# Performance work log

Hardware: AMD Instinct MI355X
Metric: run time of the kernel (lower is better)

Reference implementation:

```python
import jax, jax.numpy as jnp
import numpy as np
from jax import lax

ORDER = 6
WN = 0.5 / 50.0          # highpass_cutoff / (orig_fs/2)
UP, DOWN = 16, 25        # 64/100 reduced by gcd 4 (scipy resample_poly)
HALF_LEN = 10 * DOWN     # scipy kaiser half length = 10*max_rate
NTAPS = 2 * HALF_LEN + 1
PADLEN = 21              # sosfiltfilt default: 3*(2*n_sections+1), 3 biquads
CHANNELS = np.array([126, 125, 48, 112, 67, 93, 10, 61, 39, 108])
D_MODEL = 16
LN_EPS = 1e-5


def _butter_hp_sos(order, wn):
    # scipy.signal.butter(order, wn, btype='high', output='sos') in pure numpy
    fs = 2.0
    warped = 2.0 * fs * np.tan(np.pi * wn / fs)
    m = np.arange(-order + 1, order, 2)
    p = -np.exp(1j * np.pi * m / (2 * order))     # analog LP prototype poles
    k = np.real(1.0 / np.prod(-p))                # lp2hp gain (no zeros)
    p = warped / p                                # lp2hp poles; zeros at s=0
    z = np.zeros(order)
    fs2 = 2.0 * fs                                # bilinear, fs=2
    k = k * np.real(np.prod(fs2 - z) / np.prod(fs2 - p))
    z = (fs2 + z) / (fs2 - z)                     # digital zeros, all +1
    p = (fs2 + p) / (fs2 - p)
    pp = p[np.imag(p) > 0]
    pp = pp[np.argsort(-np.abs(np.abs(pp) - 1.0))]  # closest to unit circle last
    sos = []
    for i, pi in enumerate(pp):
        b = np.array([1.0, -2.0, 1.0]) * (k if i == 0 else 1.0)
        a = np.array([1.0, -2.0 * pi.real, np.abs(pi) ** 2])
        sos.append(np.concatenate([b, a]))
    return np.array(sos)


def _sosfilt_zi(sos):
    # scipy.signal.sosfilt_zi: steady-state of step response per section
    n = sos.shape[0]
    zi = np.zeros((n, 2))
    scale = 1.0
    for s in range(n):
        b0, b1, b2, _, a1, a2 = sos[s]
        A = np.array([[1.0 + a1, -1.0], [a2, 1.0]])
        B = np.array([b1 - a1 * b0, b2 - a2 * b0])
        zi[s] = scale * np.linalg.solve(A, B)
        scale *= (b0 + b1 + b2) / (1.0 + a1 + a2)
    return zi


SOS = _butter_hp_sos(ORDER, WN)
ZI = _sosfilt_zi(SOS)


def _resample_fir():
    # scipy firwin(2*half_len+1, 1/max_rate, window=('kaiser',5.0)) * up
    fc = 1.0 / DOWN
    m = np.arange(NTAPS) - (NTAPS - 1) / 2.0
    h = fc * np.sinc(fc * m) * np.kaiser(NTAPS, 5.0)
    h /= h.sum()
    return h * UP


H_BASE = _resample_fir()


def _pos_encoding(max_len, d):
    pos = np.arange(max_len)[:, None].astype(np.float64)
    div = np.exp(np.arange(0, d, 2) * (-np.log(10000.0) / d))
    pe = np.zeros((max_len, d))
    pe[:, 0::2] = np.sin(pos * div)
    pe[:, 1::2] = np.cos(pos * div)
    return pe.astype(np.float32)


PE = _pos_encoding(3840, D_MODEL)


def _sosfilt(x, zi):
    # x: (N,T), zi: (N,3,2). Cascade of biquads, transposed direct form II.
    sos = jnp.asarray(SOS, x.dtype)
    nsec = SOS.shape[0]

    def step(z, xt):
        v = xt
        zs = []
        for s in range(nsec):  # fixed tiny cascade, unrolled inside scan
            b0, b1, b2, a1, a2 = sos[s, 0], sos[s, 1], sos[s, 2], sos[s, 4], sos[s, 5]
            y = b0 * v + z[s][0]
            zs.append((b1 * v - a1 * y + z[s][1], b2 * v - a2 * y))
            v = y
        return tuple(zs), v

    z0 = tuple((zi[:, s, 0], zi[:, s, 1]) for s in range(nsec))
    _, y = lax.scan(step, z0, x.T)
    return y.T


def _sosfiltfilt(x):
    # scipy.signal.sosfiltfilt with default odd padding, padlen=21
    zi = jnp.asarray(ZI, x.dtype)
    front = 2.0 * x[:, :1] - x[:, PADLEN:0:-1]
    back = 2.0 * x[:, -1:] - x[:, -2:-PADLEN - 2:-1]
    ext = jnp.concatenate([front, x, back], axis=1)
    y = _sosfilt(ext, zi[None] * ext[:, 0, None, None])
    y = y[:, ::-1]
    y = _sosfilt(y, zi[None] * y[:, 0, None, None])
    return y[:, ::-1][:, PADLEN:-PADLEN]


def _resample_poly(x):
    # scipy.signal.resample_poly(x, 64, 100): upfirdn via dilated conv
    T = x.shape[-1]
    n_out = (T * UP) // DOWN + int((T * UP) % DOWN != 0)
    n_pre_pad = DOWN - HALF_LEN % DOWN
    n_pre_remove = (HALF_LEN + n_pre_pad) // DOWN

    def outlen(lh):
        return (((T - 1) * UP + lh) - 1) // DOWN + 1

    n_post = 0
    while outlen(NTAPS + n_pre_pad + n_post) < n_out + n_pre_remove:
        n_post += 1
    h = np.concatenate([np.zeros(n_pre_pad), H_BASE, np.zeros(n_post)])
    L = h.size
    rhs = jnp.asarray(h[::-1].copy(), x.dtype).reshape(1, 1, L)
    y = lax.conv_general_dilated(x[:, None, :], rhs, window_strides=(DOWN,),
                                 padding=[(L - 1, L - 1)], lhs_dilation=(UP,),
                                 dimension_numbers=('NCH', 'OIH', 'NCH'))
    return y[:, 0, n_pre_remove:n_pre_remove + n_out]


def _ln(x, g, b):
    mu = x.mean(-1, keepdims=True)
    var = ((x - mu) ** 2).mean(-1, keepdims=True)
    return (x - mu) * lax.rsqrt(var + LN_EPS) * g + b


def setup_inputs() -> dict:
    key = jax.random.key(0)
    ks = jax.random.split(key, 20)
    f32 = jnp.float32
    d = {
        'x': jax.random.normal(ks[0], (64, 128, 2000), f32),
        'conv_w': jax.random.normal(ks[1], (16, 10, 3), f32) * 0.15,
        'conv_b': jnp.zeros((16,), f32),
        'ln0_g': jnp.ones((16,), f32), 'ln0_b': jnp.zeros((16,), f32),
        'wqkv': jax.random.normal(ks[2], (48, 16), f32) * 0.125,
        'bqkv': jnp.zeros((48,), f32),
        'wo': jax.random.normal(ks[3], (16, 16), f32) * 0.25,
        'bo': jnp.zeros((16,), f32),
        'w1': jax.random.normal(ks[4], (32, 16), f32) * 0.2,
        'b1': jnp.zeros((32,), f32),
        'w2': jax.random.normal(ks[5], (16, 32), f32) * 0.2,
        'b2': jnp.zeros((16,), f32),
        'ln1_g': jnp.ones((16,), f32), 'ln1_b': jnp.zeros((16,), f32),
        'ln2_g': jnp.ones((16,), f32), 'ln2_b': jnp.zeros((16,), f32),
        'wfc': jax.random.normal(ks[6], (1, 16), f32) * 0.3,
        'bfc': jnp.zeros((1,), f32),
    }
    return d


def reference(x, conv_w, conv_b, ln0_g, ln0_b, wqkv, bqkv, wo, bo,
              w1, b1, w2, b2, ln1_g, ln1_b, ln2_g, ln2_b, wfc, bfc):
    B = x.shape[0]
    # remove Cz (last channel) then gather interesting channels
    x = x[:, :-1, :][:, jnp.asarray(CHANNELS), :]        # (B,10,T)
    x = x - x.mean(axis=1, keepdims=True)                # CAR
    C, T = x.shape[1], x.shape[2]
    xf = _sosfiltfilt(x.reshape(B * C, T))               # zero-phase highpass
    xr = _resample_poly(xf)                              # 100 Hz -> 64 Hz
    x = xr.reshape(B, C, -1)
    x = jnp.tanh(x)                                      # artifact_scale = 1.0
    mean = x.mean(axis=2, keepdims=True)                 # zscore, unbiased std
    var = ((x - mean) ** 2).sum(axis=2, keepdims=True) / (x.shape[2] - 1)
    std = jnp.maximum(jnp.sqrt(var), 1e-6)
    x = (x - mean) / std
    # conv1d k=3 pad=1 (10 -> 16) + relu
    x = lax.conv_general_dilated(x, conv_w, (1,), [(1, 1)],
                                 dimension_numbers=('NCH', 'OIH', 'NCH'))
    x = jax.nn.relu(x + conv_b[None, :, None])
    x = x.transpose(0, 2, 1)                             # (B,S,16)
    x = _ln(x, ln0_g, ln0_b)
    x = x + jnp.asarray(PE[:x.shape[1]], x.dtype)[None]
    # TransformerEncoderLayer, post-norm, nhead=1, relu FFN (eval: no dropout)
    qkv = x @ wqkv.T + bqkv
    q, k, v = jnp.split(qkv, 3, axis=-1)
    att = jax.nn.softmax(jnp.einsum('bqd,bkd->bqk', q, k) * 0.25, axis=-1)
    a = jnp.einsum('bqk,bkd->bqd', att, v) @ wo.T + bo
    x = _ln(x + a, ln1_g, ln1_b)
    f = jax.nn.relu(x @ w1.T + b1) @ w2.T + b2
    x = _ln(x + f, ln2_g, ln2_b)
    pooled = x.mean(axis=1)                              # adaptive avg pool -> 1
    return pooled @ wfc.T + bfc                          # (B,1)
```

## Files before the change

### kernel.cpp

```cpp
#include <hip/hip_runtime.h>
#include <cmath>
#include <complex>
#include <algorithm>

#ifndef M_PI
#define M_PI 3.14159265358979323846
#endif

typedef _Float16 f16x8 __attribute__((ext_vector_type(8)));
typedef _Float16 f16x4 __attribute__((ext_vector_type(4)));
typedef float f32x4 __attribute__((ext_vector_type(4)));

struct FiltArg {
  double b0[3], b1[3], b2[3], a1[3], a2[3];
  double zi0[3], zi1[3];
};
struct CorArg { double CA[16 * 6]; };
struct EigArg {
  double Pm[36], Pinv[36];
  double czi[6];
  double lam_re[3], lam_im[3];
  double lami_re[3], lami_im[3];
};
struct FirArg { float h[526]; };

static void design_sos(FiltArg& sa) {
  const int order = 6;
  const double wn = 0.5 / 50.0;
  const double fs = 2.0;
  double warped = 2.0 * fs * std::tan(M_PI * wn / fs);
  std::complex<double> p[6];
  for (int i = 0; i < order; i++) {
    int m = -order + 1 + 2 * i;
    p[i] = -std::exp(std::complex<double>(0.0, M_PI * m / (2.0 * order)));
  }
  std::complex<double> prod1(1, 0);
  for (int i = 0; i < 6; i++) prod1 *= -p[i];
  double k = (1.0 / prod1).real();
  for (int i = 0; i < 6; i++) p[i] = warped / p[i];
  const double fs2 = 2.0 * fs;
  std::complex<double> num(1, 0), den(1, 0);
  for (int i = 0; i < 6; i++) { num *= fs2; den *= (fs2 - p[i]); }
  k *= (num / den).real();
  for (int i = 0; i < 6; i++) p[i] = (fs2 + p[i]) / (fs2 - p[i]);
  std::complex<double> pp[3]; int n = 0;
  for (int i = 0; i < 6; i++) if (p[i].imag() > 0) pp[n++] = p[i];
  std::stable_sort(pp, pp + 3,
    [](const std::complex<double>& A, const std::complex<double>& B) {
      return std::fabs(std::abs(A) - 1.0) > std::fabs(std::abs(B) - 1.0);
    });
  double sos[3][6];
  for (int s = 0; s < 3; s++) {
    double g = (s == 0) ? k : 1.0;
    sos[s][0] = g; sos[s][1] = -2.0 * g; sos[s][2] = g;
    sos[s][3] = 1.0; sos[s][4] = -2.0 * pp[s].real(); sos[s][5] = std::norm(pp[s]);
  }
  double scale = 1.0;
  for (int s = 0; s < 3; s++) {
    double b0 = sos[s][0], b1 = sos[s][1], b2 = sos[s][2];
    double a1 = sos[s][4], a2 = sos[s][5];
    double det = 1.0 + a1 + a2;
    double r0 = b1 - a1 * b0, r1 = b2 - a2 * b0;
    double z0 = (r0 + r1) / det;
    double z1 = ((1.0 + a1) * r1 - a2 * r0) / det;
    sa.b0[s] = b0; sa.b1[s] = b1; sa.b2[s] = b2; sa.a1[s] = a1; sa.a2[s] = a2;
    sa.zi0[s] = scale * z0; sa.zi1[s] = scale * z1;
    scale *= (b0 + b1 + b2) / (1.0 + a1 + a2);
  }
}

static double host_step(const FiltArg& c, double z[6], double v) {
  for (int s = 0; s < 3; s++) {
    double y = c.b0[s] * v + z[2 * s];
    z[2 * s]     = c.b1[s] * v - c.a1[s] * y + z[2 * s + 1];
    z[2 * s + 1] = c.b2[s] * v - c.a2[s] * y;
    v = y;
  }
  return v;
}

static void build_filt(FiltArg& c, CorArg& co) {
  design_sos(c);
  for (int j = 0; j < 6; j++) {
    double z[6] = {0, 0, 0, 0, 0, 0};
    z[j] = 1.0;
    for (int i = 0; i < 16; i++) co.CA[i * 6 + j] = host_step(c, z, 0.0);
  }
}

static void build_eig(const FiltArg& c, EigArg& e) {
  double Pr[36];
  for (int s = 0; s < 3; s++) {
    double a1 = c.a1[s], a2 = c.a2[s];
    std::complex<double> disc = std::sqrt(std::complex<double>(a1 * a1 - 4.0 * a2, 0.0));
    std::complex<double> p = (-a1 + disc) / 2.0;
    if (p.imag() < 0) p = std::conj(p);
    std::complex<double> v[6] = {0, 0, 0, 0, 0, 0};
    v[2 * s] = 1.0;
    v[2 * s + 1] = a1 + p;
    std::complex<double> y = 1.0;
    for (int j = s + 1; j < 3; j++) {
      double b0j = c.b0[j], b1j = c.b1[j], b2j = c.b2[j];
      double a1j = c.a1[j], a2j = c.a2[j];
      std::complex<double> det = p * p + a1j * p + a2j;
      std::complex<double> r0 = (b1j - a1j * b0j) * y;
      std::complex<double> r1 = (b2j - a2j * b0j) * y;
      std::complex<double> z0 = (p * r0 + r1) / det;
      std::complex<double> z1 = ((p + a1j) * r1 - a2j * r0) / det;
      v[2 * j] = z0; v[2 * j + 1] = z1;
      y = b0j * y + z0;
    }
    for (int i = 0; i < 6; i++) {
      Pr[i * 6 + 2 * s]     = v[i].real();
      Pr[i * 6 + 2 * s + 1] = v[i].imag();
    }
    std::complex<double> lam = std::pow(p, 16);
    e.lam_re[s] = lam.real(); e.lam_im[s] = lam.imag();
    std::complex<double> li = 1.0 / lam;
    e.lami_re[s] = li.real(); e.lami_im[s] = li.imag();
  }
  for (int i = 0; i < 36; i++) e.Pm[i] = Pr[i];
  double M[6][12];
  for (int i = 0; i < 6; i++)
    for (int j = 0; j < 6; j++) { M[i][j] = Pr[i * 6 + j]; M[i][6 + j] = (i == j) ? 1.0 : 0.0; }
  for (int col = 0; col < 6; col++) {
    int piv = col;
    for (int i = col + 1; i < 6; i++)
      if (std::fabs(M[i][col]) > std::fabs(M[piv][col])) piv = i;
    if (piv != col) for (int j = 0; j < 12; j++) std::swap(M[col][j], M[piv][j]);
    double d = M[col][col];
    for (int j = 0; j < 12; j++) M[col][j] /= d;
    for (int i = 0; i < 6; i++) if (i != col) {
      double f = M[i][col];
      for (int j = 0; j < 12; j++) M[i][j] -= f * M[col][j];
    }
  }
  for (int i = 0; i < 6; i++)
    for (int j = 0; j < 6; j++) e.Pinv[i * 6 + j] = M[i][6 + j];
  double zv[6];
  for (int s = 0; s < 3; s++) { zv[2 * s] = c.zi0[s]; zv[2 * s + 1] = c.zi1[s]; }
  for (int i = 0; i < 6; i++) {
    double sum = 0.0;
    for (int j = 0; j < 6; j++) sum += e.Pinv[i * 6 + j] * zv[j];
    e.czi[i] = sum;
  }
}

static double bessel_i0(double x) {
  double s = 1.0, t = 1.0;
  for (int k = 1; k < 64; k++) {
    double u = x / (2.0 * k);
    t *= u * u; s += t;
    if (t < 1e-18 * s) break;
  }
  return s;
}

static void design_fir(FirArg& fa) {
  double h[501];
  const double fc = 1.0 / 25.0;
  double denom = bessel_i0(5.0);
  double sum = 0.0;
  for (int nn = 0; nn < 501; nn++) {
    double m = nn - 250.0;
    double xx = fc * m;
    double snc = (nn == 250) ? 1.0 : std::sin(M_PI * xx) / (M_PI * xx);
    double r = (2.0 * nn) / 500.0 - 1.0;
    double w = bessel_i0(5.0 * std::sqrt(std::max(0.0, 1.0 - r * r))) / denom;
    h[nn] = fc * snc * w; sum += h[nn];
  }
  for (int nn = 0; nn < 25; nn++) fa.h[nn] = 0.0f;
  for (int nn = 0; nn < 501; nn++) fa.h[25 + nn] = (float)(h[nn] / sum * 16.0);
}

__device__ inline double waveReduceSum(double v) {
  #pragma unroll
  for (int off = 32; off > 0; off >>= 1) v += __shfl_down(v, off, 64);
  return v;
}

__device__ inline void cpow_int(double br, double bi, int n, double& rr_, double& ri_) {
  double rr = 1.0, ri = 0.0;
  while (n) {
    if (n & 1) { double t = rr * br - ri * bi; ri = rr * bi + ri * br; rr = t; }
    double t2 = br * br - bi * bi; bi = 2.0 * br * bi; br = t2;
    n >>= 1;
  }
  rr_ = rr; ri_ = ri;
}

__global__ __launch_bounds__(256) void k_chansel_pe(const float* __restrict__ x,
                                                    float* __restrict__ xs,
                                                    float* __restrict__ pe,
                                                    float* __restrict__ out) {
  int gid = blockIdx.x;
  if (gid < 500) {
    int idx = gid * 256 + threadIdx.x;
    int b = idx / 2000, t = idx % 2000;
    const int ch[10] = {126, 125, 48, 112, 67, 93, 10, 61, 39, 108};
    const float* xb = x + (size_t)b * 128 * 2000;
    float v[10]; float s = 0.f;
    #pragma unroll
    for (int c = 0; c < 10; c++) { v[c] = xb[ch[c] * 2000 + t]; s += v[c]; }
    s *= 0.1f;
    #pragma unroll
    for (int c = 0; c < 10; c++) xs[((size_t)b * 10 + c) * 2000 + t] = v[c] - s;
  } else {
    int i = (gid - 500) * 256 + threadIdx.x;
    int t = i >> 4, d = i & 15, j = d >> 1;
    double div = exp(-((double)(2 * j)) * 0.5756462732485114);
    double a = (double)t * div;
    pe[i] = (float)((d & 1) ? cos(a) : sin(a));
    if (gid == 579 && threadIdx.x < 64) out[threadIdx.x] = 0.f;
  }
}

#define XR(t) xr[(t) + ((t) >> 5)]
#define YF(t) yf[(t) + ((t) >> 5)]
__global__ __launch_bounds__(128) void k_filtfilt(float* __restrict__ xs,
                                                  FiltArg c, CorArg co, EigArg eg) {
  __shared__ float xr[2112];
  __shared__ double yf[2112];
  __shared__ double wsum[3][2];
  int r = blockIdx.x;
  int gk = threadIdx.x;
  int lane = gk & 63;
  int wv = gk >> 6;
  float* x = xs + (size_t)r * 2000;

  float x0f = x[0], xlf = x[1999];
  for (int t = gk; t < 2048; t += 128) {
    float v;
    if (t < 21)        v = 2.f * x0f - x[21 - t];
    else if (t < 2021) v = x[t - 21];
    else if (t < 2042) v = 2.f * xlf - x[4019 - t];
    else               v = 0.f;
    XR(t) = v;
  }
  __syncthreads();

  double b0[3], b1[3], b2[3], a1[3], a2[3];
  #pragma unroll
  for (int s = 0; s < 3; s++) {
    b0[s] = c.b0[s]; b1[s] = c.b1[s]; b2[s] = c.b2[s];
    a1[s] = c.a1[s]; a2[s] = c.a2[s];
  }
  auto step = [&](double* z, double v) -> double {
    #pragma unroll
    for (int s = 0; s < 3; s++) {
      double y = b0[s] * v + z[2 * s];
      z[2 * s]     = b1[s] * v - a1[s] * y + z[2 * s + 1];
      z[2 * s + 1] = b2[s] * v - a2[s] * y;
      v = y;
    }
    return v;
  };

  auto eigscan = [&](double seed, const double* F, double* zst) {
    double G[6];
    #pragma unroll
    for (int i = 0; i < 6; i++) {
      double s = 0.0;
      #pragma unroll
      for (int j = 0; j < 6; j++) s += eg.Pinv[i * 6 + j] * F[j];
      G[i] = s;
    }
    double tre[3], tim[3], sre[3], sim[3];
    #pragma unroll
    for (int s3 = 0; s3 < 3; s3++) {
      double gre = G[2 * s3], gim = -G[2 * s3 + 1];
      double mre, mim;
      cpow_int(eg.lami_re[s3], eg.lami_im[s3], gk, mre, mim);
      tre[s3] = mre * gre - mim * gim;
      tim[s3] = mre * gim + mim * gre;
      double pr = tre[s3], pi = tim[s3];
      #pragma unroll
      for (int off = 1; off < 64; off <<= 1) {
        double ore = __shfl_up(pr, off, 64);
        double oim = __shfl_up(pi, off, 64);
        pr += (lane >= off) ? ore : 0.0;
        pi += (lane >= off) ? oim : 0.0;
      }
      sre[s3] = pr; sim[s3] = pi;
      if (wv == 0 && lane == 63) { wsum[s3][0] = pr; wsum[s3][1] = pi; }
    }
    __syncthreads();
    double coord[6];
    #pragma unroll
    for (int s3 = 0; s3 < 3; s3++) {
      double inc_re = sre[s3] + (wv ? wsum[s3][0] : 0.0);
      double inc_im = sim[s3] + (wv ? wsum[s3][1] : 0.0);
      double Sre = inc_re - tre[s3], Sim = inc_im - tim[s3];
      double c0re = seed * eg.czi[2 * s3];
      double c0im = -seed * eg.czi[2 * s3 + 1];
      double lkre, lkim;
      cpow_int(eg.lam_re[s3], eg.lam_im[s3], gk, lkre, lkim);
      double lm1re = lkre * eg.lami_re[s3] - lkim * eg.lami_im[s3];
      double lm1im = lkre * eg.lami_im[s3] + lkim * eg.lami_re[s3];
      if (gk == 0) { lm1re = 0.0; lm1im = 0.0; }
      double cre = lkre * c0re - lkim * c0im + lm1re * Sre - lm1im * Sim;
      double cim = lkre * c0im + lkim * c0re + lm1re * Sim + lm1im * Sre;
      coord[2 * s3] = cre;
      coord[2 * s3 + 1] = -cim;
    }
    #pragma unroll
    for (int i = 0; i < 6; i++) {
      double s = 0.0;
      #pragma unroll
      for (int j = 0; j < 6; j++) s += eg.Pm[i * 6 + j] * coord[j];
      zst[i] = s;
    }
  };

  int t0 = gk * 16;
  double z[6], yreg[16], zst[6];

  #pragma unroll
  for (int i = 0; i < 6; i++) z[i] = 0.0;
  for (int i = 0; i < 16; i++) yreg[i] = step(z, (double)XR(t0 + i));
  eigscan((double)XR(0), z, zst);
  for (int i = 0; i < 16; i++) {
    double corr = 0.0;
    #pragma unroll
    for (int j = 0; j < 6; j++) corr += co.CA[i * 6 + j] * zst[j];
    YF(t0 + i) = yreg[i] + corr;
  }
  __syncthreads();

  auto rin = [&](int j) -> double { return (j <= 2041) ? YF(2041 - j) : 0.0; };
  double seedB = YF(2041);
  #pragma unroll
  for (int i = 0; i < 6; i++) z[i] = 0.0;
  for (int i = 0; i < 16; i++) yreg[i] = step(z, rin(t0 + i));
  eigscan(seedB, z, zst);
  for (int i = 0; i < 16; i++) {
    int j = t0 + i;
    if (j >= 21 && j <= 2020) {
      double corr = 0.0;
      #pragma unroll
      for (int jj = 0; jj < 6; jj++) corr += co.CA[i * 6 + jj] * zst[jj];
      x[2020 - j] = (float)(yreg[i] + corr);
    }
  }
}

__global__ __launch_bounds__(256) void k_resample_norm(const float* __restrict__ xf,
                                                       float* __restrict__ xn,
                                                       FirArg fa) {
  __shared__ float xl[2000];
  __shared__ float hl[526];
  int r = blockIdx.x;
  const float* x = xf + (size_t)r * 2000;
  for (int i = threadIdx.x; i < 2000; i += 256) xl[i] = x[i];
  for (int i = threadIdx.x; i < 526; i += 256) hl[i] = fa.h[i];
  __syncthreads();
  float vals[5];
  #pragma unroll
  for (int kk = 0; kk < 5; kk++) {
    int o = threadIdx.x + kk * 256;
    int P = 25 * (o + 11);
    int phase = P & 15;
    float acc = 0.f;
    for (int m = phase; m <= 525; m += 16) {
      int idx = (P - m) >> 4;
      if (idx >= 0 && idx < 2000) acc += hl[m] * xl[idx];
    }
    vals[kk] = tanhf(acc);
  }
  double s = 0.0, ss = 0.0;
  #pragma unroll
  for (int kk = 0; kk < 5; kk++) {
    s += (double)vals[kk]; ss += (double)vals[kk] * (double)vals[kk];
  }
  s = waveReduceSum(s); ss = waveReduceSum(ss);
  __shared__ double red[8];
  int wid = threadIdx.x >> 6, lane = threadIdx.x & 63;
  if (lane == 0) { red[wid] = s; red[4 + wid] = ss; }
  __syncthreads();
  double S = red[0] + red[1] + red[2] + red[3];
  double SS = red[4] + red[5] + red[6] + red[7];
  double mean = S / 1280.0;
  double var = (SS - 1280.0 * mean * mean) / 1279.0;
  double sd = fmax(sqrt(fmax(var, 0.0)), 1e-6);
  float fmean = (float)mean, finv = (float)(1.0 / sd);
  #pragma unroll
  for (int kk = 0; kk < 5; kk++)
    xn[(size_t)r * 1280 + threadIdx.x + kk * 256] = (vals[kk] - fmean) * finv;
}

__global__ __launch_bounds__(256) void k_conv_ln_pe_qkv(const float* __restrict__ xn,
    const float* __restrict__ cw, const float* __restrict__ cb,
    const float* __restrict__ g0, const float* __restrict__ bt0,
    const float* __restrict__ wqkv, const float* __restrict__ bqkv,
    const float* __restrict__ pe,
    float* __restrict__ x0, float* __restrict__ Q,
    _Float16* __restrict__ Kp, _Float16* __restrict__ Vt_g) {
  __shared__ float w[480], bias[16], gg[16], gb[16];
  __shared__ float wq[768], bq[48];
  for (int i = threadIdx.x; i < 480; i += 256) w[i] = cw[i];
  for (int i = threadIdx.x; i < 768; i += 256) wq[i] = wqkv[i];
  if (threadIdx.x < 16) {
    bias[threadIdx.x] = cb[threadIdx.x];
    gg[threadIdx.x] = g0[threadIdx.x];
    gb[threadIdx.x] = bt0[threadIdx.x];
  }
  if (threadIdx.x < 48) bq[threadIdx.x] = bqkv[threadIdx.x];
  __syncthreads();
  int idx = blockIdx.x * 256 + threadIdx.x;
  int b = idx / 1280, t = idx % 1280;
  const float* xb = xn + (size_t)b * 10 * 1280;
  float in[10][3];
  #pragma unroll
  for (int i = 0; i < 10; i++)
    #pragma unroll
    for (int k = 0; k < 3; k++) {
      int tt = t - 1 + k;
      in[i][k] = (tt >= 0 && tt < 1280) ? xb[i * 1280 + tt] : 0.f;
    }
  float o[16];
  #pragma unroll
  for (int oc = 0; oc < 16; oc++) {
    float a = bias[oc];
    #pragma unroll
    for (int i = 0; i < 10; i++)
      #pragma unroll
      for (int k = 0; k < 3; k++) a += in[i][k] * w[oc * 30 + i * 3 + k];
    o[oc] = fmaxf(a, 0.f);
  }
  float mu = 0.f;
  #pragma unroll
  for (int d = 0; d < 16; d++) mu += o[d];
  mu *= (1.f / 16.f);
  float var = 0.f;
  #pragma unroll
  for (int d = 0; d < 16; d++) { float dd = o[d] - mu; var += dd * dd; }
  var *= (1.f / 16.f);
  float inv = 1.f / sqrtf(var + 1e-5f);
  float xv[16];
  float* outp = x0 + (size_t)idx * 16;
  const float* pep = pe + t * 16;
  #pragma unroll
  for (int d = 0; d < 16; d++) {
    xv[d] = (o[d] - mu) * inv * gg[d] + gb[d] + pep[d];
    outp[d] = xv[d];
  }
  float* qp = Q + (size_t)idx * 16;
  #pragma unroll
  for (int j = 0; j < 16; j++) {
    float a = bq[j];
    #pragma unroll
    for (int d = 0; d < 16; d++) a += xv[d] * wq[j * 16 + d];
    qp[j] = a;
  }
  {
    _Float16* kp = Kp + (size_t)idx * 32;
    #pragma unroll
    for (int j = 0; j < 16; j++) {
      float a = bq[16 + j];
      #pragma unroll
      for (int d = 0; d < 16; d++) a += xv[d] * wq[(16 + j) * 16 + d];
      kp[j] = (_Float16)a;
    }
    f16x8 zz;
    #pragma unroll
    for (int j = 0; j < 8; j++) zz[j] = (_Float16)0.f;
    *(f16x8*)&kp[16] = zz;
    *(f16x8*)&kp[24] = zz;
  }
  {
    _Float16* vt = Vt_g + (size_t)b * 16 * 1280 + t;
    #pragma unroll
    for (int j = 0; j < 16; j++) {
      float a = bq[32 + j];
      #pragma unroll
      for (int d = 0; d < 16; d++) a += xv[d] * wq[(32 + j) * 16 + d];
      vt[j * 1280] = (_Float16)a;
    }
  }
}

#define ATT_SHIFT 12.0f
__global__ __launch_bounds__(256) void k_attn_combine(const float* __restrict__ Q,
    const _Float16* __restrict__ Kp, const _Float16* __restrict__ Vt_g,
    const float* __restrict__ x0,
    const float* __restrict__ wo, const float* __restrict__ bo,
    const float* __restrict__ w1, const float* __restrict__ b1,
    const float* __restrict__ w2, const float* __restrict__ b2,
    const float* __restrict__ g1, const float* __restrict__ bb1,
    const float* __restrict__ g2, const float* __restrict__ bb2,
    const float* __restrict__ wfc, const float* __restrict__ bfc,
    float* __restrict__ out) {
  __shared__ __align__(16) _Float16 Ks2[64 * 32];
  __shared__ __align__(16) _Float16 Vt[16 * 72];
  __shared__ __align__(16) _Float16 Pld[4][16 * 40];
  __shared__ float Aly[64][17];
  __shared__ float swo[256], sw1[512], sw2[512];
  __shared__ float sbo[16], sb1[32], sb2[16], sg1[16], sbb1[16], sg2[16], sbb2[16];
  __shared__ float swf[16];
  int tid = threadIdx.x;
  int b  = blockIdx.x / 20;
  int rg = blockIdx.x % 20;
  int wv = tid >> 6;
  int lane = tid & 63;
  int col = lane & 15;
  int quad = lane >> 4;
  size_t base = (size_t)b * 1280;
  int row0 = rg * 64 + wv * 16;

  swo[tid] = wo[tid];
  for (int i = tid; i < 512; i += 256) { sw1[i] = w1[i]; sw2[i] = w2[i]; }
  if (tid < 16) {
    sbo[tid] = bo[tid]; sb2[tid] = b2[tid];
    sg1[tid] = g1[tid]; sbb1[tid] = bb1[tid];
    sg2[tid] = g2[tid]; sbb2[tid] = bb2[tid];
    swf[tid] = wfc[tid];
  }
  if (tid < 32) sb1[tid] = b1[tid];

  f16x8 qf;
  #pragma unroll
  for (int j = 0; j < 8; j++) qf[j] = (_Float16)0.f;
  if (quad < 2) {
    const float* qp = Q + (base + row0 + col) * 16 + quad * 8;
    #pragma unroll
    for (int j = 0; j < 8; j++) qf[j] = (_Float16)(0.25f * qp[j]);
  }
  f32x4 oacc = {0.f, 0.f, 0.f, 0.f};
  float lacc = 0.f;

  const _Float16* vt_b = Vt_g + (size_t)b * 16 * 1280;

  for (int s = 0; s < 20; s++) {
    __syncthreads();
    *(f16x8*)&Ks2[tid * 8] =
        *(const f16x8*)(Kp + (base + s * 64) * 32 + tid * 8);
    if (tid < 128) {
      int d = tid >> 3, qc = tid & 7;
      *(f16x8*)&Vt[d * 72 + qc * 8] =
          *(const f16x8*)(vt_b + d * 1280 + s * 64 + qc * 8);
    }
    __syncthreads();
    #pragma unroll
    for (int c = 0; c < 2; c++) {
      #pragma unroll
      for (int t = 0; t < 2; t++) {
        int keyoff = c * 32 + t * 16;
        f16x8 af = *(f16x8*)&Ks2[(keyoff + col) * 32 + quad * 8];
        f32x4 sf = {0.f, 0.f, 0.f, 0.f};
        sf = __builtin_amdgcn_mfma_f32_16x16x32_f16(af, qf, sf, 0, 0, 0);
        f16x4 ph;
        float psum = 0.f;
        #pragma unroll
        for (int r = 0; r < 4; r++) {
          float p = __expf(sf[r] - ATT_SHIFT);
          psum += p;
          ph[r] = (_Float16)p;
        }
        lacc += psum;
        *(f16x4*)&Pld[wv][col * 40 + t * 16 + quad * 4] = ph;
      }
      __syncthreads();
      f16x8 pf = *(f16x8*)&Pld[wv][col * 40 + quad * 8];
      f16x8 vf = *(f16x8*)&Vt[col * 72 + c * 32 + quad * 8];
      oacc = __builtin_amdgcn_mfma_f32_16x16x32_f16(pf, vf, oacc, 0, 0, 0);
      __syncthreads();
    }
  }
  lacc += __shfl_xor(lacc, 16, 64);
  lacc += __shfl_xor(lacc, 32, 64);
  #pragma unroll
  for (int r = 0; r < 4; r++) {
    float lr = __shfl(lacc, quad * 4 + r, 64);
    Aly[wv * 16 + quad * 4 + r][col] = oacc[r] / lr;
  }
  __syncthreads();

  if (tid < 64) {
    int grow = rg * 64 + tid;
    size_t goff = (base + grow) * 16;
    float a[16];
    #pragma unroll
    for (int d = 0; d < 16; d++) a[d] = Aly[tid][d];
    float h[16];
    const float* xr = x0 + goff;
    #pragma unroll
    for (int d = 0; d < 16; d++) {
      float o = sbo[d];
      #pragma unroll
      for (int e = 0; e < 16; e++) o += a[e] * swo[d * 16 + e];
      h[d] = xr[d] + o;
    }
    float mu = 0.f;
    #pragma unroll
    for (int d = 0; d < 16; d++) mu += h[d];
    mu *= (1.f / 16.f);
    float var = 0.f;
    #pragma unroll
    for (int d = 0; d < 16; d++) { float dd = h[d] - mu; var += dd * dd; }
    var *= (1.f / 16.f);
    float inv = 1.f / sqrtf(var + 1e-5f);
    float x1[16];
    #pragma unroll
    for (int d = 0; d < 16; d++) x1[d] = (h[d] - mu) * inv * sg1[d] + sbb1[d];
    float t1[32];
    #pragma unroll
    for (int j = 0; j < 32; j++) {
      float u = sb1[j];
      #pragma unroll
      for (int d = 0; d < 16; d++) u += x1[d] * sw1[j * 16 + d];
      t1[j] = fmaxf(u, 0.f);
    }
    float h2[16];
    #pragma unroll
    for (int d = 0; d < 16; d++) {
      float u = sb2[d];
      #pragma unroll
      for (int j = 0; j < 32; j++) u += t1[j] * sw2[d * 32 + j];
      h2[d] = x1[d] + u;
    }
    mu = 0.f;
    #pragma unroll
    for (int d = 0; d < 16; d++) mu += h2[d];
    mu *= (1.f / 16.f);
    var = 0.f;
    #pragma unroll
    for (int d = 0; d < 16; d++) { float dd = h2[d] - mu; var += dd * dd; }
    var *= (1.f / 16.f);
    inv = 1.f / sqrtf(var + 1e-5f);
    float pv = 0.f;
    #pragma unroll
    for (int d = 0; d < 16; d++)
      pv += ((h2[d] - mu) * inv * sg2[d] + sbb2[d]) * swf[d];
    double part = waveReduceSum((double)pv);
    if (tid == 0) {
      float add = (float)(part / 1280.0);
      if (blockIdx.x % 20 == 0) add += bfc[0];
      atomicAdd(&out[b], add);
    }
  }
}

extern "C" void kernel_launch(void* const* d_in, const int* in_sizes, int n_in,
                              void* d_out, int out_size, void* d_ws, size_t ws_size,
                              hipStream_t stream) {
  const float* x    = (const float*)d_in[0];
  const float* cw   = (const float*)d_in[1];
  const float* cb   = (const float*)d_in[2];
  const float* g0   = (const float*)d_in[3];
  const float* bt0  = (const float*)d_in[4];
  const float* wqkv = (const float*)d_in[5];
  const float* bqkv = (const float*)d_in[6];
  const float* wo   = (const float*)d_in[7];
  const float* bo   = (const float*)d_in[8];
  const float* w1   = (const float*)d_in[9];
  const float* b1   = (const float*)d_in[10];
  const float* w2   = (const float*)d_in[11];
  const float* b2   = (const float*)d_in[12];
  const float* g1   = (const float*)d_in[13];
  const float* bb1  = (const float*)d_in[14];
  const float* g2   = (const float*)d_in[15];
  const float* bb2  = (const float*)d_in[16];
  const float* wfc  = (const float*)d_in[17];
  const float* bfc  = (const float*)d_in[18];
  float* out = (float*)d_out;

  float* ws = (float*)d_ws;
  float* xs = ws;
  float* y1 = xs + 1280000;
  float* xn = y1 + 1306880;
  float* x0 = xn + 819200;
  float* Q  = x0 + 1310720;
  _Float16* Kp   = (_Float16*)(Q + 1310720);
  _Float16* Vt_g = (_Float16*)(Q + 2621440);
  float* pe = Q + 2621440 + 655360;

  FiltArg fc; CorArg co; EigArg eg; FirArg fa;
  build_filt(fc, co);
  build_eig(fc, eg);
  design_fir(fa);

  k_chansel_pe<<<580, 256, 0, stream>>>(x, xs, pe, out);
  k_filtfilt<<<640, 128, 0, stream>>>(xs, fc, co, eg);
  k_resample_norm<<<640, 256, 0, stream>>>(xs, xn, fa);
  k_conv_ln_pe_qkv<<<320, 256, 0, stream>>>(xn, cw, cb, g0, bt0, wqkv, bqkv,
                                            pe, x0, Q, Kp, Vt_g);
  k_attn_combine<<<1280, 256, 0, stream>>>(Q, Kp, Vt_g, x0, wo, bo, w1, b1,
                                           w2, b2, g1, bb1, g2, bb2, wfc, bfc,
                                           out);
}
```

Before: 230.8 us.

## Load attention K/V fragments directly from global and drop block barriers

Each wave now reads its K and V MFMA fragments straight from global memory into registers instead of staging them through shared memory with block-wide barriers. The four score MFMAs per 64-key tile are issued together, and the per-wave P buffer is widened so all four chunks are written before the PV MFMAs, so none of the barriers inside the loop are needed. This removes the synchronisation and LDS staging cost, but each wave now loads K/V redundantly from global or L2, and the P tile is written and read within a wave without an explicit barrier.

```diff
diff --git a/kernel.cpp b/kernel.cpp
--- a/kernel.cpp
+++ b/kernel.cpp
@@ -490,9 +490,7 @@
     const float* __restrict__ g2, const float* __restrict__ bb2,
     const float* __restrict__ wfc, const float* __restrict__ bfc,
     float* __restrict__ out) {
-  __shared__ __align__(16) _Float16 Ks2[64 * 32];
-  __shared__ __align__(16) _Float16 Vt[16 * 72];
-  __shared__ __align__(16) _Float16 Pld[4][16 * 40];
+  __shared__ __align__(16) _Float16 Pld[4][16 * 72];
   __shared__ float Aly[64][17];
   __shared__ float swo[256], sw1[512], sw2[512];
   __shared__ float sbo[16], sb1[32], sb2[16], sg1[16], sbb1[16], sg2[16], sbb2[16];
@@ -528,42 +526,53 @@
   f32x4 oacc = {0.f, 0.f, 0.f, 0.f};
   float lacc = 0.f;
 
+  const _Float16* kp_b = Kp + base * 32;
   const _Float16* vt_b = Vt_g + (size_t)b * 16 * 1280;
+  _Float16* pld = &Pld[wv][0];
+
+  f16x8 af0, af1, af2, af3;
+  #pragma unroll
+  for (int j = 0; j < 8; j++) {
+    af0[j] = (_Float16)0.f; af1[j] = (_Float16)0.f;
+    af2[j] = (_Float16)0.f; af3[j] = (_Float16)0.f;
+  }
 
   for (int s = 0; s < 20; s++) {
-    __syncthreads();
-    *(f16x8*)&Ks2[tid * 8] =
-        *(const f16x8*)(Kp + (base + s * 64) * 32 + tid * 8);
-    if (tid < 128) {
-      int d = tid >> 3, qc = tid & 7;
-      *(f16x8*)&Vt[d * 72 + qc * 8] =
-          *(const f16x8*)(vt_b + d * 1280 + s * 64 + qc * 8);
-    }
-    __syncthreads();
+    const _Float16* kt = kp_b + (size_t)s * 64 * 32;
+    if (quad < 2) {
+      af0 = *(const f16x8*)(kt + (col     ) * 32 + quad * 8);
+      af1 = *(const f16x8*)(kt + (col + 16) * 32 + quad * 8);
+      af2 = *(const f16x8*)(kt + (col + 32) * 32 + quad * 8);
+      af3 = *(const f16x8*)(kt + (col + 48) * 32 + quad * 8);
+    }
+    f16x8 vf0 = *(const f16x8*)(vt_b + col * 1280 + s * 64      + quad * 8);
+    f16x8 vf1 = *(const f16x8*)(vt_b + col * 1280 + s * 64 + 32 + quad * 8);
+
+    f32x4 sc[4];
+    #pragma unroll
+    for (int ch = 0; ch < 4; ch++) { sc[ch][0]=0.f; sc[ch][1]=0.f; sc[ch][2]=0.f; sc[ch][3]=0.f; }
+    sc[0] = __builtin_amdgcn_mfma_f32_16x16x32_f16(af0, qf, sc[0], 0, 0, 0);
+    sc[1] = __builtin_amdgcn_mfma_f32_16x16x32_f16(af1, qf, sc[1], 0, 0, 0);
+    sc[2] = __builtin_amdgcn_mfma_f32_16x16x32_f16(af2, qf, sc[2], 0, 0, 0);
+    sc[3] = __builtin_amdgcn_mfma_f32_16x16x32_f16(af3, qf, sc[3], 0, 0, 0);
+
+    #pragma unroll
+    for (int ch = 0; ch < 4; ch++) {
+      f16x4 ph; float psum = 0.f;
+      #pragma unroll
+      for (int r = 0; r < 4; r++) {
+        float p = __expf(sc[ch][r] - ATT_SHIFT);
+        psum += p;
+        ph[r] = (_Float16)p;
+      }
+      lacc += psum;
+      *(f16x4*)&pld[col * 72 + ch * 16 + quad * 4] = ph;
+    }
     #pragma unroll
     for (int c = 0; c < 2; c++) {
-      #pragma unroll
-      for (int t = 0; t < 2; t++) {
-        int keyoff = c * 32 + t * 16;
-        f16x8 af = *(f16x8*)&Ks2[(keyoff + col) * 32 + quad * 8];
-        f32x4 sf = {0.f, 0.f, 0.f, 0.f};
-        sf = __builtin_amdgcn_mfma_f32_16x16x32_f16(af, qf, sf, 0, 0, 0);
-        f16x4 ph;
-        float psum = 0.f;
-        #pragma unroll
-        for (int r = 0; r < 4; r++) {
-          float p = __expf(sf[r] - ATT_SHIFT);
-          psum += p;
-          ph[r] = (_Float16)p;
-        }
-        lacc += psum;
-        *(f16x4*)&Pld[wv][col * 40 + t * 16 + quad * 4] = ph;
-      }
-      __syncthreads();
-      f16x8 pf = *(f16x8*)&Pld[wv][col * 40 + quad * 8];
-      f16x8 vf = *(f16x8*)&Vt[col * 72 + c * 32 + quad * 8];
-      oacc = __builtin_amdgcn_mfma_f32_16x16x32_f16(pf, vf, oacc, 0, 0, 0);
-      __syncthreads();
+      f16x8 pf = *(f16x8*)&pld[col * 72 + c * 32 + quad * 8];
+      oacc = __builtin_amdgcn_mfma_f32_16x16x32_f16(pf, (c == 0) ? vf0 : vf1,
+                                                    oacc, 0, 0, 0);
     }
   }
   lacc += __shfl_xor(lacc, 16, 64);
```

New measurement: 243.0 us. +5.3%, slower.

## Split attention keys across waves with 32x32 MFMA and register-prefetched K/V

Applied to the files above, without the earlier changes.

Attention is restructured so each of the four waves covers all 64 query rows of the block but only a quarter of the keys. Scores come from 32x32x16 MFMAs, and K/V fragments are read straight from global memory into registers with one-step prefetch, replacing the shared-memory staging and the block-wide barriers. Partial outputs and row sums are then reduced across waves through shared memory. Q is now stored pre-scaled in fp16 and K is stored unpadded (16 halves per row instead of 32), which halves the K traffic and drops the zero-fill writes. The cost is more shared memory per block (larger P buffers plus per-wave partial outputs), which may lower occupancy.

```diff
diff --git a/kernel.cpp b/kernel.cpp
--- a/kernel.cpp
+++ b/kernel.cpp
@@ -10,6 +10,7 @@
 typedef _Float16 f16x8 __attribute__((ext_vector_type(8)));
 typedef _Float16 f16x4 __attribute__((ext_vector_type(4)));
 typedef float f32x4 __attribute__((ext_vector_type(4)));
+typedef float f32x16 __attribute__((ext_vector_type(16)));
 
 struct FiltArg {
   double b0[3], b1[3], b2[3], a1[3], a2[3];
@@ -393,7 +394,7 @@
     const float* __restrict__ g0, const float* __restrict__ bt0,
     const float* __restrict__ wqkv, const float* __restrict__ bqkv,
     const float* __restrict__ pe,
-    float* __restrict__ x0, float* __restrict__ Q,
+    float* __restrict__ x0, _Float16* __restrict__ Qh,
     _Float16* __restrict__ Kp, _Float16* __restrict__ Vt_g) {
   __shared__ float w[480], bias[16], gg[16], gb[16];
   __shared__ float wq[768], bq[48];
@@ -444,16 +445,16 @@
     xv[d] = (o[d] - mu) * inv * gg[d] + gb[d] + pep[d];
     outp[d] = xv[d];
   }
-  float* qp = Q + (size_t)idx * 16;
+  _Float16* qh = Qh + (size_t)idx * 16;
   #pragma unroll
   for (int j = 0; j < 16; j++) {
     float a = bq[j];
     #pragma unroll
     for (int d = 0; d < 16; d++) a += xv[d] * wq[j * 16 + d];
-    qp[j] = a;
+    qh[j] = (_Float16)(0.25f * a);
   }
   {
-    _Float16* kp = Kp + (size_t)idx * 32;
+    _Float16* kp = Kp + (size_t)idx * 16;
     #pragma unroll
     for (int j = 0; j < 16; j++) {
       float a = bq[16 + j];
@@ -461,11 +462,6 @@
       for (int d = 0; d < 16; d++) a += xv[d] * wq[(16 + j) * 16 + d];
       kp[j] = (_Float16)a;
     }
-    f16x8 zz;
-    #pragma unroll
-    for (int j = 0; j < 8; j++) zz[j] = (_Float16)0.f;
-    *(f16x8*)&kp[16] = zz;
-    *(f16x8*)&kp[24] = zz;
   }
   {
     _Float16* vt = Vt_g + (size_t)b * 16 * 1280 + t;
@@ -480,7 +476,7 @@
 }
 
 #define ATT_SHIFT 12.0f
-__global__ __launch_bounds__(256) void k_attn_combine(const float* __restrict__ Q,
+__global__ __launch_bounds__(256) void k_attn_combine(const _Float16* __restrict__ Qh,
     const _Float16* __restrict__ Kp, const _Float16* __restrict__ Vt_g,
     const float* __restrict__ x0,
     const float* __restrict__ wo, const float* __restrict__ bo,
@@ -490,10 +486,9 @@
     const float* __restrict__ g2, const float* __restrict__ bb2,
     const float* __restrict__ wfc, const float* __restrict__ bfc,
     float* __restrict__ out) {
-  __shared__ __align__(16) _Float16 Ks2[64 * 32];
-  __shared__ __align__(16) _Float16 Vt[16 * 72];
-  __shared__ __align__(16) _Float16 Pld[4][16 * 40];
-  __shared__ float Aly[64][17];
+  __shared__ __align__(16) _Float16 Pld[4][64 * 40];
+  __shared__ float AlyW[4][64][17];
+  __shared__ float Lly[4][64];
   __shared__ float swo[256], sw1[512], sw2[512];
   __shared__ float sbo[16], sb1[32], sb2[16], sg1[16], sbb1[16], sg2[16], sbb2[16];
   __shared__ float swf[16];
@@ -502,10 +497,12 @@
   int rg = blockIdx.x % 20;
   int wv = tid >> 6;
   int lane = tid & 63;
+  int l31 = lane & 31;
+  int lh = lane >> 5;
   int col = lane & 15;
   int quad = lane >> 4;
   size_t base = (size_t)b * 1280;
-  int row0 = rg * 64 + wv * 16;
+  int qrow0 = rg * 64;
 
   swo[tid] = wo[tid];
   for (int i = tid; i < 512; i += 256) { sw1[i] = w1[i]; sw2[i] = w2[i]; }
@@ -517,70 +514,85 @@
   }
   if (tid < 32) sb1[tid] = b1[tid];
 
-  f16x8 qf;
-  #pragma unroll
-  for (int j = 0; j < 8; j++) qf[j] = (_Float16)0.f;
-  if (quad < 2) {
-    const float* qp = Q + (base + row0 + col) * 16 + quad * 8;
-    #pragma unroll
-    for (int j = 0; j < 8; j++) qf[j] = (_Float16)(0.25f * qp[j]);
-  }
-  f32x4 oacc = {0.f, 0.f, 0.f, 0.f};
-  float lacc = 0.f;
-
+  f16x8 qf0 = *(const f16x8*)(Qh + (base + qrow0 + l31) * 16 + lh * 8);
+  f16x8 qf1 = *(const f16x8*)(Qh + (base + qrow0 + 32 + l31) * 16 + lh * 8);
+
+  const _Float16* kp_b = Kp + base * 16;
   const _Float16* vt_b = Vt_g + (size_t)b * 16 * 1280;
-
-  for (int s = 0; s < 20; s++) {
-    __syncthreads();
-    *(f16x8*)&Ks2[tid * 8] =
-        *(const f16x8*)(Kp + (base + s * 64) * 32 + tid * 8);
-    if (tid < 128) {
-      int d = tid >> 3, qc = tid & 7;
-      *(f16x8*)&Vt[d * 72 + qc * 8] =
-          *(const f16x8*)(vt_b + d * 1280 + s * 64 + qc * 8);
-    }
-    __syncthreads();
-    #pragma unroll
-    for (int c = 0; c < 2; c++) {
-      #pragma unroll
-      for (int t = 0; t < 2; t++) {
-        int keyoff = c * 32 + t * 16;
-        f16x8 af = *(f16x8*)&Ks2[(keyoff + col) * 32 + quad * 8];
-        f32x4 sf = {0.f, 0.f, 0.f, 0.f};
-        sf = __builtin_amdgcn_mfma_f32_16x16x32_f16(af, qf, sf, 0, 0, 0);
-        f16x4 ph;
-        float psum = 0.f;
+  int key0 = wv * 320;
+  _Float16* pld = &Pld[wv][0];
+
+  f32x4 oacc[4];
+  #pragma unroll
+  for (int mp = 0; mp < 4; mp++) { oacc[mp][0]=0.f; oacc[mp][1]=0.f; oacc[mp][2]=0.f; oacc[mp][3]=0.f; }
+  float lacc0 = 0.f, lacc1 = 0.f;
+
+  f16x8 afc0 = *(const f16x8*)(kp_b + (size_t)(key0 + l31) * 16 + lh * 8);
+  f16x8 afc1 = *(const f16x8*)(kp_b + (size_t)(key0 + 32 + l31) * 16 + lh * 8);
+  f16x8 vfc0 = *(const f16x8*)(vt_b + (size_t)col * 1280 + key0 + quad * 8);
+  f16x8 vfc1 = *(const f16x8*)(vt_b + (size_t)col * 1280 + key0 + 32 + quad * 8);
+
+  for (int t = 0; t < 5; t++) {
+    f16x8 afn0, afn1, vfn0, vfn1;
+    if (t < 4) {
+      int nk = key0 + (t + 1) * 64;
+      afn0 = *(const f16x8*)(kp_b + (size_t)(nk + l31) * 16 + lh * 8);
+      afn1 = *(const f16x8*)(kp_b + (size_t)(nk + 32 + l31) * 16 + lh * 8);
+      vfn0 = *(const f16x8*)(vt_b + (size_t)col * 1280 + nk + quad * 8);
+      vfn1 = *(const f16x8*)(vt_b + (size_t)col * 1280 + nk + 32 + quad * 8);
+    }
+    #pragma unroll
+    for (int ks = 0; ks < 2; ks++) {
+      f16x8 af = ks ? afc1 : afc0;
+      f16x8 vf = ks ? vfc1 : vfc0;
+      f32x16 sc0, sc1;
+      #pragma unroll
+      for (int i = 0; i < 16; i++) { sc0[i] = 0.f; sc1[i] = 0.f; }
+      sc0 = __builtin_amdgcn_mfma_f32_32x32x16_f16(af, qf0, sc0, 0, 0, 0);
+      sc1 = __builtin_amdgcn_mfma_f32_32x32x16_f16(af, qf1, sc1, 0, 0, 0);
+      #pragma unroll
+      for (int g = 0; g < 4; g++) {
+        f16x4 p0, p1; float ps0 = 0.f, ps1 = 0.f;
         #pragma unroll
         for (int r = 0; r < 4; r++) {
-          float p = __expf(sf[r] - ATT_SHIFT);
-          psum += p;
-          ph[r] = (_Float16)p;
+          float e0 = __expf(sc0[4 * g + r] - ATT_SHIFT);
+          float e1 = __expf(sc1[4 * g + r] - ATT_SHIFT);
+          ps0 += e0; ps1 += e1;
+          p0[r] = (_Float16)e0; p1[r] = (_Float16)e1;
         }
-        lacc += psum;
-        *(f16x4*)&Pld[wv][col * 40 + t * 16 + quad * 4] = ph;
+        lacc0 += ps0; lacc1 += ps1;
+        int kl = g * 8 + lh * 4;
+        *(f16x4*)&pld[l31 * 40 + kl]        = p0;
+        *(f16x4*)&pld[(32 + l31) * 40 + kl] = p1;
       }
-      __syncthreads();
-      f16x8 pf = *(f16x8*)&Pld[wv][col * 40 + quad * 8];
-      f16x8 vf = *(f16x8*)&Vt[col * 72 + c * 32 + quad * 8];
-      oacc = __builtin_amdgcn_mfma_f32_16x16x32_f16(pf, vf, oacc, 0, 0, 0);
-      __syncthreads();
-    }
-  }
-  lacc += __shfl_xor(lacc, 16, 64);
-  lacc += __shfl_xor(lacc, 32, 64);
-  #pragma unroll
-  for (int r = 0; r < 4; r++) {
-    float lr = __shfl(lacc, quad * 4 + r, 64);
-    Aly[wv * 16 + quad * 4 + r][col] = oacc[r] / lr;
-  }
+      #pragma unroll
+      for (int mp = 0; mp < 4; mp++) {
+        f16x8 pf = *(f16x8*)&pld[(mp * 16 + col) * 40 + quad * 8];
+        oacc[mp] = __builtin_amdgcn_mfma_f32_16x16x32_f16(pf, vf, oacc[mp], 0, 0, 0);
+      }
+    }
+    if (t < 4) { afc0 = afn0; afc1 = afn1; vfc0 = vfn0; vfc1 = vfn1; }
+  }
+
+  lacc0 += __shfl_xor(lacc0, 32, 64);
+  lacc1 += __shfl_xor(lacc1, 32, 64);
+  if (lane < 32) { Lly[wv][lane] = lacc0; Lly[wv][32 + lane] = lacc1; }
+  #pragma unroll
+  for (int mp = 0; mp < 4; mp++)
+    #pragma unroll
+    for (int r = 0; r < 4; r++)
+      AlyW[wv][mp * 16 + quad * 4 + r][col] = oacc[mp][r];
   __syncthreads();
 
   if (tid < 64) {
+    float lt = Lly[0][tid] + Lly[1][tid] + Lly[2][tid] + Lly[3][tid];
+    float linv = 1.f / lt;
     int grow = rg * 64 + tid;
     size_t goff = (base + grow) * 16;
     float a[16];
     #pragma unroll
-    for (int d = 0; d < 16; d++) a[d] = Aly[tid][d];
+    for (int d = 0; d < 16; d++)
+      a[d] = (AlyW[0][tid][d] + AlyW[1][tid][d] + AlyW[2][tid][d] + AlyW[3][tid][d]) * linv;
     float h[16];
     const float* xr = x0 + goff;
     #pragma unroll
@@ -669,10 +681,10 @@
   float* y1 = xs + 1280000;
   float* xn = y1 + 1306880;
   float* x0 = xn + 819200;
-  float* Q  = x0 + 1310720;
-  _Float16* Kp   = (_Float16*)(Q + 1310720);
-  _Float16* Vt_g = (_Float16*)(Q + 2621440);
-  float* pe = Q + 2621440 + 655360;
+  _Float16* Qh   = (_Float16*)(x0 + 1310720);
+  _Float16* Kp   = (_Float16*)(x0 + 1310720 + 655360);
+  _Float16* Vt_g = (_Float16*)(x0 + 1310720 + 2 * 655360);
+  float* pe = x0 + 1310720 + 3 * 655360;
 
   FiltArg fc; CorArg co; EigArg eg; FirArg fa;
   build_filt(fc, co);
@@ -683,8 +695,8 @@
   k_filtfilt<<<640, 128, 0, stream>>>(xs, fc, co, eg);
   k_resample_norm<<<640, 256, 0, stream>>>(xs, xn, fa);
   k_conv_ln_pe_qkv<<<320, 256, 0, stream>>>(xn, cw, cb, g0, bt0, wqkv, bqkv,
-                                            pe, x0, Q, Kp, Vt_g);
-  k_attn_combine<<<1280, 256, 0, stream>>>(Q, Kp, Vt_g, x0, wo, bo, w1, b1,
+                                            pe, x0, Qh, Kp, Vt_g);
+  k_attn_combine<<<1280, 256, 0, stream>>>(Qh, Kp, Vt_g, x0, wo, bo, w1, b1,
                                            w2, b2, g1, bb1, g2, bb2, wfc, bfc,
                                            out);
 }
```

After: 237.0 us. +2.7%, slower.

## Double-buffer attention K/V tiles, drop per-chunk barriers, compute row sums via MFMA

Applied to the files above, without the earlier changes.

The attention kernel now loads 128-key K/V tiles into double-buffered shared memory, prefetching the next tile into registers while the current one is processed. This cuts the loop to one barrier per tile instead of several per 32-key chunk. Q is stored as pre-scaled fp16 (folding 1/sqrt(d) and log2e) so exp2 can be used, and K is stored unpadded at 16 halves per row. The softmax denominator is accumulated with an MFMA against a ones vector instead of shuffles. This trades some fp16 rounding of Q and of the row sums, plus more shared memory, for less synchronisation and less global traffic.

```diff
diff --git a/kernel.cpp b/kernel.cpp
--- a/kernel.cpp
+++ b/kernel.cpp
@@ -9,6 +9,7 @@
 
 typedef _Float16 f16x8 __attribute__((ext_vector_type(8)));
 typedef _Float16 f16x4 __attribute__((ext_vector_type(4)));
+typedef __fp16 fp16x2 __attribute__((ext_vector_type(2)));
 typedef float f32x4 __attribute__((ext_vector_type(4)));
 
 struct FiltArg {
@@ -393,7 +394,7 @@
     const float* __restrict__ g0, const float* __restrict__ bt0,
     const float* __restrict__ wqkv, const float* __restrict__ bqkv,
     const float* __restrict__ pe,
-    float* __restrict__ x0, float* __restrict__ Q,
+    float* __restrict__ x0, _Float16* __restrict__ Qh,
     _Float16* __restrict__ Kp, _Float16* __restrict__ Vt_g) {
   __shared__ float w[480], bias[16], gg[16], gb[16];
   __shared__ float wq[768], bq[48];
@@ -444,16 +445,16 @@
     xv[d] = (o[d] - mu) * inv * gg[d] + gb[d] + pep[d];
     outp[d] = xv[d];
   }
-  float* qp = Q + (size_t)idx * 16;
+  _Float16* qh = Qh + (size_t)idx * 16;
   #pragma unroll
   for (int j = 0; j < 16; j++) {
     float a = bq[j];
     #pragma unroll
     for (int d = 0; d < 16; d++) a += xv[d] * wq[j * 16 + d];
-    qp[j] = a;
+    qh[j] = (_Float16)(0.36067376f * a);
   }
   {
-    _Float16* kp = Kp + (size_t)idx * 32;
+    _Float16* kp = Kp + (size_t)idx * 16;
     #pragma unroll
     for (int j = 0; j < 16; j++) {
       float a = bq[16 + j];
@@ -461,11 +462,6 @@
       for (int d = 0; d < 16; d++) a += xv[d] * wq[(16 + j) * 16 + d];
       kp[j] = (_Float16)a;
     }
-    f16x8 zz;
-    #pragma unroll
-    for (int j = 0; j < 8; j++) zz[j] = (_Float16)0.f;
-    *(f16x8*)&kp[16] = zz;
-    *(f16x8*)&kp[24] = zz;
   }
   {
     _Float16* vt = Vt_g + (size_t)b * 16 * 1280 + t;
@@ -479,8 +475,8 @@
   }
 }
 
-#define ATT_SHIFT 12.0f
-__global__ __launch_bounds__(256) void k_attn_combine(const float* __restrict__ Q,
+#define SHIFT2 17.3123404907f
+__global__ __launch_bounds__(256) void k_attn_combine(const _Float16* __restrict__ Qh,
     const _Float16* __restrict__ Kp, const _Float16* __restrict__ Vt_g,
     const float* __restrict__ x0,
     const float* __restrict__ wo, const float* __restrict__ bo,
@@ -490,8 +486,8 @@
     const float* __restrict__ g2, const float* __restrict__ bb2,
     const float* __restrict__ wfc, const float* __restrict__ bfc,
     float* __restrict__ out) {
-  __shared__ __align__(16) _Float16 Ks2[64 * 32];
-  __shared__ __align__(16) _Float16 Vt[16 * 72];
+  __shared__ __align__(16) _Float16 Ks[2][128 * 16];
+  __shared__ __align__(16) _Float16 Vt[2][16 * 136];
   __shared__ __align__(16) _Float16 Pld[4][16 * 40];
   __shared__ float Aly[64][17];
   __shared__ float swo[256], sw1[512], sw2[512];
@@ -520,59 +516,77 @@
   f16x8 qf;
   #pragma unroll
   for (int j = 0; j < 8; j++) qf[j] = (_Float16)0.f;
-  if (quad < 2) {
-    const float* qp = Q + (base + row0 + col) * 16 + quad * 8;
-    #pragma unroll
-    for (int j = 0; j < 8; j++) qf[j] = (_Float16)(0.25f * qp[j]);
-  }
+  if (quad < 2)
+    qf = *(const f16x8*)(Qh + (base + row0 + col) * 16 + quad * 8);
+
+  f16x8 ones;
+  #pragma unroll
+  for (int j = 0; j < 8; j++) ones[j] = (_Float16)1.f;
+
+  const _Float16* kp_b = Kp + base * 16;
+  const _Float16* vt_b = Vt_g + (size_t)b * 16 * 1280;
+  _Float16* pld = &Pld[wv][0];
+
+  int srow = tid >> 1, shalf = tid & 1;
+  int sd = tid >> 4, sseg = tid & 15;
+
+  {
+    f16x8 kreg = *(const f16x8*)(kp_b + (size_t)srow * 16 + shalf * 8);
+    f16x8 vreg = *(const f16x8*)(vt_b + (size_t)sd * 1280 + sseg * 8);
+    *(f16x8*)&Ks[0][srow * 16 + shalf * 8] = kreg;
+    *(f16x8*)&Vt[0][sd * 136 + sseg * 8] = vreg;
+  }
+
   f32x4 oacc = {0.f, 0.f, 0.f, 0.f};
-  float lacc = 0.f;
-
-  const _Float16* vt_b = Vt_g + (size_t)b * 16 * 1280;
-
-  for (int s = 0; s < 20; s++) {
+  f32x4 lacc = {0.f, 0.f, 0.f, 0.f};
+
+  for (int s = 0; s < 10; s++) {
+    int cur = s & 1;
+    f16x8 kreg, vreg;
+    if (s < 9) {
+      kreg = *(const f16x8*)(kp_b + (size_t)((s + 1) * 128 + srow) * 16 + shalf * 8);
+      vreg = *(const f16x8*)(vt_b + (size_t)sd * 1280 + (s + 1) * 128 + sseg * 8);
+    }
     __syncthreads();
-    *(f16x8*)&Ks2[tid * 8] =
-        *(const f16x8*)(Kp + (base + s * 64) * 32 + tid * 8);
-    if (tid < 128) {
-      int d = tid >> 3, qc = tid & 7;
-      *(f16x8*)&Vt[d * 72 + qc * 8] =
-          *(const f16x8*)(vt_b + d * 1280 + s * 64 + qc * 8);
-    }
-    __syncthreads();
-    #pragma unroll
-    for (int c = 0; c < 2; c++) {
+    const _Float16* ks = &Ks[cur][0];
+    const _Float16* vt = &Vt[cur][0];
+    #pragma unroll
+    for (int c = 0; c < 4; c++) {
       #pragma unroll
       for (int t = 0; t < 2; t++) {
         int keyoff = c * 32 + t * 16;
-        f16x8 af = *(f16x8*)&Ks2[(keyoff + col) * 32 + quad * 8];
-        f32x4 sf = {0.f, 0.f, 0.f, 0.f};
+        f16x8 af;
+        #pragma unroll
+        for (int j = 0; j < 8; j++) af[j] = (_Float16)0.f;
+        if (quad < 2)
+          af = *(const f16x8*)&ks[(keyoff + col) * 16 + quad * 8];
+        f32x4 sf = {-SHIFT2, -SHIFT2, -SHIFT2, -SHIFT2};
         sf = __builtin_amdgcn_mfma_f32_16x16x32_f16(af, qf, sf, 0, 0, 0);
+        float e0 = __builtin_amdgcn_exp2f(sf[0]);
+        float e1 = __builtin_amdgcn_exp2f(sf[1]);
+        float e2 = __builtin_amdgcn_exp2f(sf[2]);
+        float e3 = __builtin_amdgcn_exp2f(sf[3]);
+        fp16x2 lo = __builtin_amdgcn_cvt_pkrtz(e0, e1);
+        fp16x2 hi = __builtin_amdgcn_cvt_pkrtz(e2, e3);
         f16x4 ph;
-        float psum = 0.f;
-        #pragma unroll
-        for (int r = 0; r < 4; r++) {
-          float p = __expf(sf[r] - ATT_SHIFT);
-          psum += p;
-          ph[r] = (_Float16)p;
-        }
-        lacc += psum;
-        *(f16x4*)&Pld[wv][col * 40 + t * 16 + quad * 4] = ph;
+        ph[0] = (_Float16)lo[0]; ph[1] = (_Float16)lo[1];
+        ph[2] = (_Float16)hi[0]; ph[3] = (_Float16)hi[1];
+        *(f16x4*)&pld[col * 40 + t * 16 + quad * 4] = ph;
       }
-      __syncthreads();
-      f16x8 pf = *(f16x8*)&Pld[wv][col * 40 + quad * 8];
-      f16x8 vf = *(f16x8*)&Vt[col * 72 + c * 32 + quad * 8];
+      f16x8 pf = *(f16x8*)&pld[col * 40 + quad * 8];
+      f16x8 vf = *(const f16x8*)&vt[col * 136 + c * 32 + quad * 8];
       oacc = __builtin_amdgcn_mfma_f32_16x16x32_f16(pf, vf, oacc, 0, 0, 0);
-      __syncthreads();
-    }
-  }
-  lacc += __shfl_xor(lacc, 16, 64);
-  lacc += __shfl_xor(lacc, 32, 64);
-  #pragma unroll
-  for (int r = 0; r < 4; r++) {
-    float lr = __shfl(lacc, quad * 4 + r, 64);
-    Aly[wv * 16 + quad * 4 + r][col] = oacc[r] / lr;
-  }
+      lacc = __builtin_amdgcn_mfma_f32_16x16x32_f16(pf, ones, lacc, 0, 0, 0);
+    }
+    if (s < 9) {
+      *(f16x8*)&Ks[cur ^ 1][srow * 16 + shalf * 8] = kreg;
+      *(f16x8*)&Vt[cur ^ 1][sd * 136 + sseg * 8] = vreg;
+    }
+  }
+
+  #pragma unroll
+  for (int r = 0; r < 4; r++)
+    Aly[wv * 16 + quad * 4 + r][col] = oacc[r] / lacc[r];
   __syncthreads();
 
   if (tid < 64) {
@@ -669,10 +683,10 @@
   float* y1 = xs + 1280000;
   float* xn = y1 + 1306880;
   float* x0 = xn + 819200;
-  float* Q  = x0 + 1310720;
-  _Float16* Kp   = (_Float16*)(Q + 1310720);
-  _Float16* Vt_g = (_Float16*)(Q + 2621440);
-  float* pe = Q + 2621440 + 655360;
+  _Float16* Qh   = (_Float16*)(x0 + 1310720);
+  _Float16* Kp   = (_Float16*)(x0 + 1310720 + 655360);
+  _Float16* Vt_g = (_Float16*)(x0 + 1310720 + 2 * 655360);
+  float* pe = x0 + 1310720 + 3 * 655360;
 
   FiltArg fc; CorArg co; EigArg eg; FirArg fa;
   build_filt(fc, co);
@@ -683,8 +697,8 @@
   k_filtfilt<<<640, 128, 0, stream>>>(xs, fc, co, eg);
   k_resample_norm<<<640, 256, 0, stream>>>(xs, xn, fa);
   k_conv_ln_pe_qkv<<<320, 256, 0, stream>>>(xn, cw, cb, g0, bt0, wqkv, bqkv,
-                                            pe, x0, Q, Kp, Vt_g);
-  k_attn_combine<<<1280, 256, 0, stream>>>(Q, Kp, Vt_g, x0, wo, bo, w1, b1,
+                                            pe, x0, Qh, Kp, Vt_g);
+  k_attn_combine<<<1280, 256, 0, stream>>>(Qh, Kp, Vt_g, x0, wo, bo, w1, b1,
                                            w2, b2, g1, bb1, g2, bb2, wfc, bfc,
                                            out);
 }
```

New measurement: 233.6 us. Within noise of the previous version (+1.2%).
